# Kernel tuning notes

Measured on AMD Instinct MI355X. Metric: run time of the kernel, lower is better.

## Reference

```python
import jax, jax.numpy as jnp
import numpy as np

E, T, D, H = 8, 4096, 2048, 1024  # num_experts, tokens_per_expert, dim, hidden_dim

def setup_inputs() -> dict:
    key = jax.random.key(0)
    kx, k1, k2, k3 = jax.random.split(key, 4)
    x = jax.random.normal(kx, (E, T, D), dtype=jnp.float32)
    # trunc_normal_(std=0.02) approximated by normal*0.02 (math-equivalent scale for baseline)
    w1 = jax.random.normal(k1, (E, D, H), dtype=jnp.float32) * 0.02
    w2 = jax.random.normal(k2, (E, H, D), dtype=jnp.float32) * 0.02
    w3 = jax.random.normal(k3, (E, D, H), dtype=jnp.float32) * 0.02
    return {"x": x, "w1": w1, "w2": w2, "w3": w3}

def reference(x, w1, w2, w3):
    # GroupedExperts forward, bmm path (num_local_tokens_per_expert=None):
    # h = silu(x @ w1) * (x @ w3); out = h @ w2, batched over experts.
    h = jax.nn.silu(jnp.einsum('etd,edh->eth', x, w1))
    h = h * jnp.einsum('etd,edh->eth', x, w3)
    out = jnp.einsum('eth,ehd->etd', h, w2)
    return out
```

## Files before the change

### kernel.cpp

```cpp
#include <hip/hip_runtime.h>
#include <hip/hip_bf16.h>

#define E_    8
#define T_    4096
#define D_    2048
#define HDIM  1024

typedef __bf16 bf16_t;
typedef __bf16 bf16x8 __attribute__((ext_vector_type(8)));
typedef __bf16 bf16x4 __attribute__((ext_vector_type(4)));
typedef float  floatx4 __attribute__((ext_vector_type(4)));


__global__ void cvt_f32_bf16(const float* __restrict__ in, bf16_t* __restrict__ out, long n4) {
  long i = (long)blockIdx.x * blockDim.x + threadIdx.x;
  if (i >= n4) return;
  const float4 v = ((const float4*)in)[i];
  bf16x4 o;
  o[0] = (bf16_t)v.x; o[1] = (bf16_t)v.y; o[2] = (bf16_t)v.z; o[3] = (bf16_t)v.w;
  ((bf16x4*)out)[i] = o;
}

__global__ void transpose_cvt(const float* __restrict__ in, bf16_t* __restrict__ out,
                              int R, int C, long sIn, long sOut) {
  __shared__ float t[32][33];
  const float* inE = in + (long)blockIdx.z * sIn;
  bf16_t* outE = out + (long)blockIdx.z * sOut;
  const int tx = threadIdx.x & 31;
  const int ty = threadIdx.x >> 5;
  const int c0 = blockIdx.x * 32;
  const int r0 = blockIdx.y * 32;
#pragma unroll
  for (int j = 0; j < 4; ++j) {
    int r = ty + j * 8;
    t[r][tx] = inE[(long)(r0 + r) * C + c0 + tx];
  }
  __syncthreads();
#pragma unroll
  for (int j = 0; j < 4; ++j) {
    int c = ty + j * 8;
    outE[(long)(c0 + c) * R + r0 + tx] = (bf16_t)t[tx][c];
  }
}


__device__ __forceinline__ void async_cp16(const bf16_t* g, bf16_t* l) {
  __builtin_amdgcn_global_load_lds(
      (const __attribute__((address_space(1))) unsigned int*)(g),
      (__attribute__((address_space(3))) unsigned int*)(l), 16, 0, 0);
}

__global__ __launch_bounds__(256, 2) void gemm1_silu(
    const bf16_t* __restrict__ X, const bf16_t* __restrict__ W1t,
    const bf16_t* __restrict__ W3t, bf16_t* __restrict__ Hout,
    long sx, long sw, long sh) {
  const int K   = D_;
  const int NLD = HDIM;
  const bf16_t* A  = X   + (long)blockIdx.z * sx;
  const bf16_t* B1 = W1t + (long)blockIdx.z * sw;
  const bf16_t* B3 = W3t + (long)blockIdx.z * sw;
  bf16_t* HO = Hout + (long)blockIdx.z * sh;

  const int m0 = blockIdx.y * 128;
  const int n0 = blockIdx.x * 128;

  __shared__ bf16_t As[128 * 32];
  __shared__ bf16_t B1s[128 * 32];
  __shared__ bf16_t B3s[128 * 32];

  const int tid  = threadIdx.x;
  const int lane = tid & 63;
  const int wave = tid >> 6;
  const int wm   = (wave >> 1) * 64;
  const int wn   = (wave & 1) * 64;
  const int quad = lane >> 4;
  const int l16  = lane & 15;

  floatx4 acc1[4][4] = {};
  floatx4 acc3[4][4] = {};

  const int srow = tid >> 2;
  const int scol = (tid & 3) * 8;

  for (int k0 = 0; k0 < K; k0 += 32) {
    __syncthreads();
#pragma unroll
    for (int r = 0; r < 2; ++r) {
      const int row = r * 64 + srow;
      async_cp16(A  + (long)(m0 + row) * K + k0 + scol, As  + row * 32 + scol);
      async_cp16(B1 + (long)(n0 + row) * K + k0 + scol, B1s + row * 32 + scol);
      async_cp16(B3 + (long)(n0 + row) * K + k0 + scol, B3s + row * 32 + scol);
    }
    __syncthreads();

    bf16x8 af[4], b1f[4], b3f[4];
#pragma unroll
    for (int i = 0; i < 4; ++i)
      af[i] = *(const bf16x8*)(As + (wm + i * 16 + l16) * 32 + quad * 8);
#pragma unroll
    for (int i = 0; i < 4; ++i)
      b1f[i] = *(const bf16x8*)(B1s + (wn + i * 16 + l16) * 32 + quad * 8);
#pragma unroll
    for (int i = 0; i < 4; ++i)
      b3f[i] = *(const bf16x8*)(B3s + (wn + i * 16 + l16) * 32 + quad * 8);

#pragma unroll
    for (int i = 0; i < 4; ++i)
#pragma unroll
      for (int n = 0; n < 4; ++n) {
        acc1[i][n] = __builtin_amdgcn_mfma_f32_16x16x32_bf16(af[i], b1f[n], acc1[i][n], 0, 0, 0);
        acc3[i][n] = __builtin_amdgcn_mfma_f32_16x16x32_bf16(af[i], b3f[n], acc3[i][n], 0, 0, 0);
      }
  }

#pragma unroll
  for (int i = 0; i < 4; ++i)
#pragma unroll
    for (int n = 0; n < 4; ++n) {
      const int col = n0 + wn + n * 16 + l16;
#pragma unroll
      for (int r = 0; r < 4; ++r) {
        const int row = m0 + wm + i * 16 + quad * 4 + r;
        float g = acc1[i][n][r];
        float u = acc3[i][n][r];
        float s = g / (1.0f + __expf(-g));
        HO[(long)row * NLD + col] = (bf16_t)(s * u);
      }
    }
}

__global__ __launch_bounds__(256, 2) void gemm2(
    const bf16_t* __restrict__ Hin, const bf16_t* __restrict__ W2t,
    float* __restrict__ Out, long sh, long sw, long so) {
  const int K   = HDIM;
  const int NLD = D_;
  const bf16_t* A = Hin + (long)blockIdx.z * sh;
  const bf16_t* B = W2t + (long)blockIdx.z * sw;
  float* C = Out + (long)blockIdx.z * so;

  const int m0 = blockIdx.y * 128;
  const int n0 = blockIdx.x * 128;

  __shared__ bf16_t As[128 * 32];
  __shared__ bf16_t Bs[128 * 32];

  const int tid  = threadIdx.x;
  const int lane = tid & 63;
  const int wave = tid >> 6;
  const int wm   = (wave >> 1) * 64;
  const int wn   = (wave & 1) * 64;
  const int quad = lane >> 4;
  const int l16  = lane & 15;

  floatx4 acc[4][4] = {};

  const int srow = tid >> 2;
  const int scol = (tid & 3) * 8;

  for (int k0 = 0; k0 < K; k0 += 32) {
    __syncthreads();
#pragma unroll
    for (int r = 0; r < 2; ++r) {
      const int row = r * 64 + srow;
      async_cp16(A + (long)(m0 + row) * K + k0 + scol, As + row * 32 + scol);
      async_cp16(B + (long)(n0 + row) * K + k0 + scol, Bs + row * 32 + scol);
    }
    __syncthreads();

    bf16x8 af[4], bf[4];
#pragma unroll
    for (int i = 0; i < 4; ++i)
      af[i] = *(const bf16x8*)(As + (wm + i * 16 + l16) * 32 + quad * 8);
#pragma unroll
    for (int i = 0; i < 4; ++i)
      bf[i] = *(const bf16x8*)(Bs + (wn + i * 16 + l16) * 32 + quad * 8);

#pragma unroll
    for (int i = 0; i < 4; ++i)
#pragma unroll
      for (int n = 0; n < 4; ++n)
        acc[i][n] = __builtin_amdgcn_mfma_f32_16x16x32_bf16(af[i], bf[n], acc[i][n], 0, 0, 0);
  }

#pragma unroll
  for (int i = 0; i < 4; ++i)
#pragma unroll
    for (int n = 0; n < 4; ++n) {
      const int col = n0 + wn + n * 16 + l16;
#pragma unroll
      for (int r = 0; r < 4; ++r) {
        const int row = m0 + wm + i * 16 + quad * 4 + r;
        C[(long)row * NLD + col] = acc[i][n][r];
      }
    }
}


extern "C" void kernel_launch(void* const* d_in, const int* in_sizes, int n_in,
                              void* d_out, int out_size, void* d_ws, size_t ws_size,
                              hipStream_t stream) {
  const float* x  = (const float*)d_in[0];
  const float* w1 = (const float*)d_in[1];
  const float* w2 = (const float*)d_in[2];
  const float* w3 = (const float*)d_in[3];
  float* out = (float*)d_out;

  bf16_t* xb = (bf16_t*)d_out;
  char* ws = (char*)d_ws;
  const long MB = 1024L * 1024L;

  {
    long n4 = (long)E_ * T_ * D_ / 4;
    cvt_f32_bf16<<<dim3((unsigned)((n4 + 255) / 256)), dim3(256), 0, stream>>>(x, xb, n4);
  }

  const long sWfull = (long)D_ * HDIM;
  if (ws_size >= (size_t)(160 * MB)) {
    bf16_t* w1t = (bf16_t*)(ws + 0 * MB);
    bf16_t* w3t = (bf16_t*)(ws + 32 * MB);
    bf16_t* w2t = (bf16_t*)(ws + 64 * MB);
    bf16_t* hbuf = (bf16_t*)(ws + 96 * MB);

    transpose_cvt<<<dim3(HDIM / 32, D_ / 32, E_), 256, 0, stream>>>(w1, w1t, D_, HDIM, sWfull, sWfull);
    transpose_cvt<<<dim3(HDIM / 32, D_ / 32, E_), 256, 0, stream>>>(w3, w3t, D_, HDIM, sWfull, sWfull);
    transpose_cvt<<<dim3(D_ / 32, HDIM / 32, E_), 256, 0, stream>>>(w2, w2t, HDIM, D_, sWfull, sWfull);

    gemm1_silu<<<dim3(HDIM / 128, T_ / 128, E_), 256, 0, stream>>>(
        xb, w1t, w3t, hbuf, (long)T_ * D_, sWfull, (long)T_ * HDIM);
    gemm2<<<dim3(D_ / 128, T_ / 128, E_), 256, 0, stream>>>(
        hbuf, w2t, out, (long)T_ * HDIM, sWfull, (long)T_ * D_);
  } else {
    bf16_t* w1t = (bf16_t*)(ws + 0 * MB);
    bf16_t* w3t = (bf16_t*)(ws + 4 * MB);
    bf16_t* w2t = (bf16_t*)(ws + 8 * MB);
    bf16_t* hbuf = (bf16_t*)(ws + 12 * MB);
    for (int e = E_ - 1; e >= 0; --e) {
      const float* w1e = w1 + (long)e * sWfull;
      const float* w3e = w3 + (long)e * sWfull;
      const float* w2e = w2 + (long)e * sWfull;
      transpose_cvt<<<dim3(HDIM / 32, D_ / 32, 1), 256, 0, stream>>>(w1e, w1t, D_, HDIM, 0, 0);
      transpose_cvt<<<dim3(HDIM / 32, D_ / 32, 1), 256, 0, stream>>>(w3e, w3t, D_, HDIM, 0, 0);
      transpose_cvt<<<dim3(D_ / 32, HDIM / 32, 1), 256, 0, stream>>>(w2e, w2t, HDIM, D_, 0, 0);
      gemm1_silu<<<dim3(HDIM / 128, T_ / 128, 1), 256, 0, stream>>>(
          xb + (long)e * T_ * D_, w1t, w3t, hbuf, 0, 0, 0);
      gemm2<<<dim3(D_ / 128, T_ / 128, 1), 256, 0, stream>>>(
          hbuf, w2t, out + (long)e * T_ * D_, 0, 0, 0);
    }
  }
}
```

Before: 1.080 ms.

## Enlarge GEMM tiles to 256 rows and add 4-stage async LDS pipeline

Both expert GEMMs move to 512-thread blocks with 256-row (and for gemm2, 256-column) tiles. Each block keeps a 4-slot ring of shared-memory K tiles filled by async global-to-LDS loads issued three tiles ahead, waited on with explicit vmcnt and raw s_barriers. MFMA bursts are split into two phases with raised wave priority so loads overlap compute. The goal is to hide memory latency and raise operand reuse per block. The cost is much more LDS per block (gemm1 about 128KB, gemm2 128KB), which likely limits occupancy to one block per CU despite the launch bound of 2.

```diff
diff --git a/kernel.cpp b/kernel.cpp
--- a/kernel.cpp
+++ b/kernel.cpp
@@ -50,147 +50,225 @@
       (__attribute__((address_space(3))) unsigned int*)(l), 16, 0, 0);
 }
 
-__global__ __launch_bounds__(256, 2) void gemm1_silu(
+__device__ __forceinline__ void phase_barrier() {
+  __builtin_amdgcn_sched_barrier(0);
+  __builtin_amdgcn_s_barrier();
+  __builtin_amdgcn_sched_barrier(0);
+}
+
+#define MFMA_BF16 __builtin_amdgcn_mfma_f32_16x16x32_bf16
+
+__global__ __launch_bounds__(512, 2) void gemm1_silu(
     const bf16_t* __restrict__ X, const bf16_t* __restrict__ W1t,
     const bf16_t* __restrict__ W3t, bf16_t* __restrict__ Hout,
     long sx, long sw, long sh) {
-  const int K   = D_;
-  const int NLD = HDIM;
+  const int K  = D_;
+  const int NT = K / 32;
   const bf16_t* A  = X   + (long)blockIdx.z * sx;
   const bf16_t* B1 = W1t + (long)blockIdx.z * sw;
   const bf16_t* B3 = W3t + (long)blockIdx.z * sw;
   bf16_t* HO = Hout + (long)blockIdx.z * sh;
 
-  const int m0 = blockIdx.y * 128;
+  const int m0 = blockIdx.y * 256;
   const int n0 = blockIdx.x * 128;
 
-  __shared__ bf16_t As[128 * 32];
-  __shared__ bf16_t B1s[128 * 32];
-  __shared__ bf16_t B3s[128 * 32];
+  __shared__ bf16_t As [4 * 256 * 32];
+  __shared__ bf16_t B1s[4 * 128 * 32];
+  __shared__ bf16_t B3s[4 * 128 * 32];
 
   const int tid  = threadIdx.x;
   const int lane = tid & 63;
   const int wave = tid >> 6;
-  const int wm   = (wave >> 1) * 64;
-  const int wn   = (wave & 1) * 64;
+  const int wm   = (wave >> 2) * 128;
+  const int wn   = (wave & 3) * 32;
   const int quad = lane >> 4;
   const int l16  = lane & 15;
 
-  floatx4 acc1[4][4] = {};
-  floatx4 acc3[4][4] = {};
-
   const int srow = tid >> 2;
   const int scol = (tid & 3) * 8;
 
-  for (int k0 = 0; k0 < K; k0 += 32) {
-    __syncthreads();
-#pragma unroll
-    for (int r = 0; r < 2; ++r) {
-      const int row = r * 64 + srow;
-      async_cp16(A  + (long)(m0 + row) * K + k0 + scol, As  + row * 32 + scol);
-      async_cp16(B1 + (long)(n0 + row) * K + k0 + scol, B1s + row * 32 + scol);
-      async_cp16(B3 + (long)(n0 + row) * K + k0 + scol, B3s + row * 32 + scol);
-    }
-    __syncthreads();
-
-    bf16x8 af[4], b1f[4], b3f[4];
-#pragma unroll
-    for (int i = 0; i < 4; ++i)
-      af[i] = *(const bf16x8*)(As + (wm + i * 16 + l16) * 32 + quad * 8);
-#pragma unroll
-    for (int i = 0; i < 4; ++i)
-      b1f[i] = *(const bf16x8*)(B1s + (wn + i * 16 + l16) * 32 + quad * 8);
-#pragma unroll
-    for (int i = 0; i < 4; ++i)
-      b3f[i] = *(const bf16x8*)(B3s + (wn + i * 16 + l16) * 32 + quad * 8);
-
-#pragma unroll
-    for (int i = 0; i < 4; ++i)
-#pragma unroll
-      for (int n = 0; n < 4; ++n) {
-        acc1[i][n] = __builtin_amdgcn_mfma_f32_16x16x32_bf16(af[i], b1f[n], acc1[i][n], 0, 0, 0);
-        acc3[i][n] = __builtin_amdgcn_mfma_f32_16x16x32_bf16(af[i], b3f[n], acc3[i][n], 0, 0, 0);
-      }
-  }
-
-#pragma unroll
-  for (int i = 0; i < 4; ++i)
-#pragma unroll
-    for (int n = 0; n < 4; ++n) {
+  const bf16_t* pa0 = A  + (long)(m0 + srow) * K + scol;
+  const bf16_t* pa1 = A  + (long)(m0 + 128 + srow) * K + scol;
+  const bf16_t* pb1 = B1 + (long)(n0 + srow) * K + scol;
+  const bf16_t* pb3 = B3 + (long)(n0 + srow) * K + scol;
+  bf16_t* la  = As  + tid * 8;
+  bf16_t* lb1 = B1s + tid * 8;
+  bf16_t* lb3 = B3s + tid * 8;
+
+  auto stageA = [&](int kt, int slot) {
+    async_cp16(pa0 + kt * 32, la + slot * 8192);
+    async_cp16(pa1 + kt * 32, la + slot * 8192 + 4096);
+  };
+  auto stageB = [&](int kt, int slot) {
+    async_cp16(pb1 + kt * 32, lb1 + slot * 4096);
+    async_cp16(pb3 + kt * 32, lb3 + slot * 4096);
+  };
+
+  floatx4 acc1[8][2] = {};
+  floatx4 acc3[8][2] = {};
+
+  stageA(0, 0); stageB(0, 0);
+  stageA(1, 1); stageB(1, 1);
+  stageA(2, 2); stageB(2, 2);
+
+  for (int t = 0; t < NT; ++t) {
+    const int c  = t & 3;
+    const int s  = (t + 3) & 3;
+    const int kp = (t + 3 < NT) ? (t + 3) : (NT - 1);
+
+    stageA(kp, s);
+    asm volatile("s_waitcnt vmcnt(10)" ::: "memory");
+    phase_barrier();
+
+    const bf16_t* Ab  = As  + c * 8192;
+    const bf16_t* Bb1 = B1s + c * 4096;
+    const bf16_t* Bb3 = B3s + c * 4096;
+
+    bf16x8 af[8];
+#pragma unroll
+    for (int i = 0; i < 8; ++i)
+      af[i] = *(const bf16x8*)(Ab + (wm + i * 16 + l16) * 32 + quad * 8);
+    bf16x8 b1a = *(const bf16x8*)(Bb1 + (wn + l16) * 32 + quad * 8);
+    bf16x8 b1b = *(const bf16x8*)(Bb1 + (wn + 16 + l16) * 32 + quad * 8);
+
+    __builtin_amdgcn_s_setprio(1);
+#pragma unroll
+    for (int i = 0; i < 8; ++i) {
+      acc1[i][0] = MFMA_BF16(af[i], b1a, acc1[i][0], 0, 0, 0);
+      acc1[i][1] = MFMA_BF16(af[i], b1b, acc1[i][1], 0, 0, 0);
+    }
+    __builtin_amdgcn_s_setprio(0);
+    phase_barrier();
+
+    bf16x8 b3a = *(const bf16x8*)(Bb3 + (wn + l16) * 32 + quad * 8);
+    bf16x8 b3b = *(const bf16x8*)(Bb3 + (wn + 16 + l16) * 32 + quad * 8);
+    stageB(kp, s);
+
+    __builtin_amdgcn_s_setprio(1);
+#pragma unroll
+    for (int i = 0; i < 8; ++i) {
+      acc3[i][0] = MFMA_BF16(af[i], b3a, acc3[i][0], 0, 0, 0);
+      acc3[i][1] = MFMA_BF16(af[i], b3b, acc3[i][1], 0, 0, 0);
+    }
+    __builtin_amdgcn_s_setprio(0);
+    phase_barrier();
+  }
+
+#pragma unroll
+  for (int i = 0; i < 8; ++i)
+#pragma unroll
+    for (int n = 0; n < 2; ++n) {
       const int col = n0 + wn + n * 16 + l16;
 #pragma unroll
       for (int r = 0; r < 4; ++r) {
         const int row = m0 + wm + i * 16 + quad * 4 + r;
         float g = acc1[i][n][r];
         float u = acc3[i][n][r];
-        float s = g / (1.0f + __expf(-g));
-        HO[(long)row * NLD + col] = (bf16_t)(s * u);
+        float sv = g / (1.0f + __expf(-g));
+        HO[(long)row * HDIM + col] = (bf16_t)(sv * u);
       }
     }
 }
 
-__global__ __launch_bounds__(256, 2) void gemm2(
+__global__ __launch_bounds__(512, 2) void gemm2(
     const bf16_t* __restrict__ Hin, const bf16_t* __restrict__ W2t,
     float* __restrict__ Out, long sh, long sw, long so) {
-  const int K   = HDIM;
-  const int NLD = D_;
+  const int K  = HDIM;
+  const int NT = K / 32;
   const bf16_t* A = Hin + (long)blockIdx.z * sh;
   const bf16_t* B = W2t + (long)blockIdx.z * sw;
   float* C = Out + (long)blockIdx.z * so;
 
-  const int m0 = blockIdx.y * 128;
-  const int n0 = blockIdx.x * 128;
-
-  __shared__ bf16_t As[128 * 32];
-  __shared__ bf16_t Bs[128 * 32];
+  const int m0 = blockIdx.y * 256;
+  const int n0 = blockIdx.x * 256;
+
+  __shared__ bf16_t As[4 * 256 * 32];
+  __shared__ bf16_t Bs[4 * 256 * 32];
 
   const int tid  = threadIdx.x;
   const int lane = tid & 63;
   const int wave = tid >> 6;
-  const int wm   = (wave >> 1) * 64;
-  const int wn   = (wave & 1) * 64;
+  const int wm   = (wave >> 2) * 128;
+  const int wn   = (wave & 3) * 64;
   const int quad = lane >> 4;
   const int l16  = lane & 15;
 
-  floatx4 acc[4][4] = {};
-
   const int srow = tid >> 2;
   const int scol = (tid & 3) * 8;
 
-  for (int k0 = 0; k0 < K; k0 += 32) {
-    __syncthreads();
-#pragma unroll
-    for (int r = 0; r < 2; ++r) {
-      const int row = r * 64 + srow;
-      async_cp16(A + (long)(m0 + row) * K + k0 + scol, As + row * 32 + scol);
-      async_cp16(B + (long)(n0 + row) * K + k0 + scol, Bs + row * 32 + scol);
-    }
-    __syncthreads();
-
-    bf16x8 af[4], bf[4];
-#pragma unroll
-    for (int i = 0; i < 4; ++i)
-      af[i] = *(const bf16x8*)(As + (wm + i * 16 + l16) * 32 + quad * 8);
-#pragma unroll
-    for (int i = 0; i < 4; ++i)
-      bf[i] = *(const bf16x8*)(Bs + (wn + i * 16 + l16) * 32 + quad * 8);
-
-#pragma unroll
-    for (int i = 0; i < 4; ++i)
-#pragma unroll
-      for (int n = 0; n < 4; ++n)
-        acc[i][n] = __builtin_amdgcn_mfma_f32_16x16x32_bf16(af[i], bf[n], acc[i][n], 0, 0, 0);
-  }
-
-#pragma unroll
-  for (int i = 0; i < 4; ++i)
+  const bf16_t* pa0 = A + (long)(m0 + srow) * K + scol;
+  const bf16_t* pa1 = A + (long)(m0 + 128 + srow) * K + scol;
+  const bf16_t* pb0 = B + (long)(n0 + srow) * K + scol;
+  const bf16_t* pb1 = B + (long)(n0 + 128 + srow) * K + scol;
+  bf16_t* la = As + tid * 8;
+  bf16_t* lb = Bs + tid * 8;
+
+  auto stageA = [&](int kt, int slot) {
+    async_cp16(pa0 + kt * 32, la + slot * 8192);
+    async_cp16(pa1 + kt * 32, la + slot * 8192 + 4096);
+  };
+  auto stageB = [&](int kt, int slot) {
+    async_cp16(pb0 + kt * 32, lb + slot * 8192);
+    async_cp16(pb1 + kt * 32, lb + slot * 8192 + 4096);
+  };
+
+  floatx4 acc[8][4] = {};
+
+  stageA(0, 0); stageB(0, 0);
+  stageA(1, 1); stageB(1, 1);
+  stageA(2, 2); stageB(2, 2);
+
+  for (int t = 0; t < NT; ++t) {
+    const int c  = t & 3;
+    const int s  = (t + 3) & 3;
+    const int kp = (t + 3 < NT) ? (t + 3) : (NT - 1);
+
+    stageA(kp, s);
+    asm volatile("s_waitcnt vmcnt(10)" ::: "memory");
+    phase_barrier();
+
+    const bf16_t* Ab = As + c * 8192;
+    const bf16_t* Bb = Bs + c * 8192;
+
+    bf16x8 af[8];
+#pragma unroll
+    for (int i = 0; i < 8; ++i)
+      af[i] = *(const bf16x8*)(Ab + (wm + i * 16 + l16) * 32 + quad * 8);
+    bf16x8 bf0 = *(const bf16x8*)(Bb + (wn + l16) * 32 + quad * 8);
+    bf16x8 bf1 = *(const bf16x8*)(Bb + (wn + 16 + l16) * 32 + quad * 8);
+
+    __builtin_amdgcn_s_setprio(1);
+#pragma unroll
+    for (int i = 0; i < 8; ++i) {
+      acc[i][0] = MFMA_BF16(af[i], bf0, acc[i][0], 0, 0, 0);
+      acc[i][1] = MFMA_BF16(af[i], bf1, acc[i][1], 0, 0, 0);
+    }
+    __builtin_amdgcn_s_setprio(0);
+    phase_barrier();
+
+    bf16x8 bf2 = *(const bf16x8*)(Bb + (wn + 32 + l16) * 32 + quad * 8);
+    bf16x8 bf3 = *(const bf16x8*)(Bb + (wn + 48 + l16) * 32 + quad * 8);
+    stageB(kp, s);
+
+    __builtin_amdgcn_s_setprio(1);
+#pragma unroll
+    for (int i = 0; i < 8; ++i) {
+      acc[i][2] = MFMA_BF16(af[i], bf2, acc[i][2], 0, 0, 0);
+      acc[i][3] = MFMA_BF16(af[i], bf3, acc[i][3], 0, 0, 0);
+    }
+    __builtin_amdgcn_s_setprio(0);
+    phase_barrier();
+  }
+
+#pragma unroll
+  for (int i = 0; i < 8; ++i)
 #pragma unroll
     for (int n = 0; n < 4; ++n) {
       const int col = n0 + wn + n * 16 + l16;
 #pragma unroll
       for (int r = 0; r < 4; ++r) {
         const int row = m0 + wm + i * 16 + quad * 4 + r;
-        C[(long)row * NLD + col] = acc[i][n][r];
+        C[(long)row * D_ + col] = acc[i][n][r];
       }
     }
 }
@@ -225,9 +303,9 @@
     transpose_cvt<<<dim3(HDIM / 32, D_ / 32, E_), 256, 0, stream>>>(w3, w3t, D_, HDIM, sWfull, sWfull);
     transpose_cvt<<<dim3(D_ / 32, HDIM / 32, E_), 256, 0, stream>>>(w2, w2t, HDIM, D_, sWfull, sWfull);
 
-    gemm1_silu<<<dim3(HDIM / 128, T_ / 128, E_), 256, 0, stream>>>(
+    gemm1_silu<<<dim3(HDIM / 128, T_ / 256, E_), 512, 0, stream>>>(
         xb, w1t, w3t, hbuf, (long)T_ * D_, sWfull, (long)T_ * HDIM);
-    gemm2<<<dim3(D_ / 128, T_ / 128, E_), 256, 0, stream>>>(
+    gemm2<<<dim3(D_ / 256, T_ / 256, E_), 512, 0, stream>>>(
         hbuf, w2t, out, (long)T_ * HDIM, sWfull, (long)T_ * D_);
   } else {
     bf16_t* w1t = (bf16_t*)(ws + 0 * MB);
@@ -241,9 +319,9 @@
       transpose_cvt<<<dim3(HDIM / 32, D_ / 32, 1), 256, 0, stream>>>(w1e, w1t, D_, HDIM, 0, 0);
       transpose_cvt<<<dim3(HDIM / 32, D_ / 32, 1), 256, 0, stream>>>(w3e, w3t, D_, HDIM, 0, 0);
       transpose_cvt<<<dim3(D_ / 32, HDIM / 32, 1), 256, 0, stream>>>(w2e, w2t, HDIM, D_, 0, 0);
-      gemm1_silu<<<dim3(HDIM / 128, T_ / 128, 1), 256, 0, stream>>>(
+      gemm1_silu<<<dim3(HDIM / 128, T_ / 256, 1), 512, 0, stream>>>(
           xb + (long)e * T_ * D_, w1t, w3t, hbuf, 0, 0, 0);
-      gemm2<<<dim3(D_ / 128, T_ / 128, 1), 256, 0, stream>>>(
+      gemm2<<<dim3(D_ / 256, T_ / 256, 1), 512, 0, stream>>>(
           hbuf, w2t, out + (long)e * T_ * D_, 0, 0, 0);
     }
   }
```

Measured after the change: 1.136 ms. 5.2% more time.
